# Kernel tuning notes

Hardware: AMD Instinct MI355X
Metric: run time of the kernel (lower is better)

## Reference

```python
import jax, jax.numpy as jnp
import numpy as np

T, D_IN, D_OUT, HEADS, FREQ = 2048, 1024, 1024, 8, 10000
DH = D_OUT // HEADS


def absolute_pos(t, d, freq):
    # AP[pos, 2i] = sin(pos / freq**(2i/d)), AP[pos, 2i+1] = cos(...); t even -> all cols filled
    pos = jnp.arange(t, dtype=jnp.float32)[:, None]            # [T,1]
    i = jnp.arange(t // 2, dtype=jnp.float32)[None, :]         # [1,T/2]
    angle = pos / (freq ** (2.0 * i / d))                      # [T,T/2]
    return jnp.stack([jnp.sin(angle), jnp.cos(angle)], axis=-1).reshape(t, t)


def setup_inputs() -> dict:
    key = jax.random.key(0)
    ks = jax.random.split(key, 6)
    s = 0.02
    return {
        "x": jax.random.normal(ks[0], (T, D_IN), jnp.float32),
        "Wq": jax.random.normal(ks[1], (HEADS, DH, D_IN), jnp.float32) * s,
        "Wk": jax.random.normal(ks[2], (HEADS, DH, D_IN), jnp.float32) * s,
        "Wv": jax.random.normal(ks[3], (HEADS, DH, D_IN), jnp.float32) * s,
        "Wout2": jax.random.normal(ks[4], (DH, DH + 2), jnp.float32) * s,
        "Wout": jax.random.normal(ks[5], (D_IN, D_OUT), jnp.float32) * s,
    }


def reference(x, Wq, Wk, Wv, Wout2, Wout):
    t = x.shape[0]
    # diversity = 1 - cosine similarity (F.normalize with eps=1e-12)
    x_unit = x / jnp.maximum(jnp.linalg.norm(x, axis=1, keepdims=True), 1e-12)
    diversity = 1.0 - x_unit @ x_unit.T                        # [T,T]

    # all heads vectorized; torch Linear weight is [out,in] -> x @ W.T
    Q = jnp.einsum('td,hed->hte', x, Wq)                       # [H,T,DH]
    K = jnp.einsum('td,hed->hte', x, Wk)
    V = jnp.einsum('td,hed->hte', x, Wv)

    AP = absolute_pos(t, D_IN, FREQ)                           # [T,T]
    energies = jnp.einsum('hte,hse->hts', Q, K) + AP           # [H,T,T]

    att = jax.nn.softmax(energies, axis=-1)
    logp = jax.nn.log_softmax(energies, axis=-1)
    entropy = -(att * logp).sum(-1) / np.float32(np.log(t))    # [H,T]
    entropy = entropy / jnp.maximum(jnp.abs(entropy).sum(-1, keepdims=True), 1e-12)

    # dep_factor[j] broadcast over rows: masked[i,j] = dep[j]*att[i,j]
    dep = (diversity[None] * att).sum(-1) / diversity.sum(-1)[None]  # [H,T]
    att_win = att + dep[:, None, :] * att                      # [H,T,T]

    # dropout(p=0.5) treated as identity (eval mode)
    y = jnp.einsum('hts,hse->hte', att_win, V)                 # [H,T,DH]

    chars = jax.lax.stop_gradient(jnp.stack([entropy, dep], axis=-1))  # [H,T,2]
    y_s = jnp.einsum('htf,of->hto', jnp.concatenate([y, chars], axis=-1), Wout2)  # [H,T,DH]

    y_cat = jnp.transpose(y_s, (1, 0, 2)).reshape(t, D_OUT)    # cat heads along feature dim
    out = y_cat @ Wout.T                                       # [T,D_IN]
    return out, att_win[-1]
```

## Files before the change

### kernel.cpp

```cpp
#include <hip/hip_runtime.h>
#include <math.h>

#define TT  2048
#define NH  8
#define DH  128
#define LNT 7.6246189861593985f

typedef unsigned short ushort_t;
typedef __bf16 bf16x8 __attribute__((ext_vector_type(8)));
typedef _Float16 f16x8 __attribute__((ext_vector_type(8)));
typedef float f32x4 __attribute__((ext_vector_type(4)));
typedef unsigned int uintx4 __attribute__((ext_vector_type(4)));

#define MFMA16(a, b, c)  __builtin_amdgcn_mfma_f32_16x16x32_bf16(a, b, c, 0, 0, 0)
#define MFMA16F(a, b, c) __builtin_amdgcn_mfma_f32_16x16x32_f16(a, b, c, 0, 0, 0)

__device__ __forceinline__ bf16x8 ld8(const ushort_t* p) {
  uintx4 v = *(const uintx4*)p;
  return __builtin_bit_cast(bf16x8, v);
}
__device__ __forceinline__ f16x8 ld8f(const ushort_t* p) {
  uintx4 v = *(const uintx4*)p;
  return __builtin_bit_cast(f16x8, v);
}
__device__ __forceinline__ ushort_t f2bf(float x) {
  unsigned u = __float_as_uint(x);
  return (ushort_t)((u + 0x7fffu + ((u >> 16) & 1u)) >> 16);
}
__device__ __forceinline__ float bf2f(ushort_t b) {
  return __uint_as_float(((unsigned)b) << 16);
}
__device__ __forceinline__ ushort_t f2h(float x) {
  return __builtin_bit_cast(ushort_t, (_Float16)x);
}
__device__ __forceinline__ float h2f(ushort_t b) {
  return (float)__builtin_bit_cast(_Float16, b);
}


enum : size_t {
  F_XF   = 0u,
  F_UF   = 1048576u,
  F_QF   = 2097152u,
  F_KF   = 3145728u,
  F_VBF  = 4194304u,
  F_VT   = 5242880u,
  F_YCF  = 6291456u,
  F_WCAT = 7340032u,
  F_WOF  = 9437184u,
  F_DIVS = 9961472u,
  F_LST  = 9979904u,
  F_ENTR = 9996288u,
  F_ENT  = 10012672u,
  F_DEP  = 10029056u,
  F_W2F  = 10307584u,
  F_APH  = 10485760u,
  F_C    = 12582912u,
  F_LP   = 6291456u,
  F_SAP  = 6422528u,
  F_SCP  = 6553600u,
  F_E    = 16777216u,
  F_YPALL= 33554432u,
  F_YSH  = 2097152u,
};

__device__ __forceinline__ float blockReduceSum256(float v) {
  __shared__ float sh[4];
  #pragma unroll
  for (int m = 1; m < 64; m <<= 1) v += __shfl_xor(v, m, 64);
  if ((threadIdx.x & 63) == 0) sh[threadIdx.x >> 6] = v;
  __syncthreads();
  float r = sh[0] + sh[1] + sh[2] + sh[3];
  __syncthreads();
  return r;
}

__global__ __launch_bounds__(256) void k_pre(
    const float* __restrict__ x, const float* __restrict__ Wq,
    const float* __restrict__ Wk, const float* __restrict__ Wv,
    const float* __restrict__ Wo, const float* __restrict__ W2,
    ushort_t* __restrict__ xf, ushort_t* __restrict__ Wcat,
    ushort_t* __restrict__ Wof, ushort_t* __restrict__ W2f,
    ushort_t* __restrict__ Uf, float* __restrict__ divsum) {
  int b = blockIdx.x;
  if (b < 4192) {
    int i = b * 256 + threadIdx.x;
    if (i < 1048576) {
      const float* src; ushort_t* dst; int j;
      if (i < 262144)       { src = Wq; dst = Wcat;           j = i; }
      else if (i < 524288)  { src = Wk; dst = Wcat + 1048576; j = i - 262144; }
      else if (i < 786432)  { src = Wv; dst = Wcat + 2097152; j = i - 524288; }
      else                  { src = Wo; dst = Wof;            j = i - 786432; }
      float4 v = ((const float4*)src)[j];
      uint2 w;
      w.x = (unsigned)f2h(v.x) | ((unsigned)f2h(v.y) << 16);
      w.y = (unsigned)f2h(v.z) | ((unsigned)f2h(v.w) << 16);
      ((uint2*)dst)[j] = w;
    } else {
      int idx = i - 1048576;
      int o = idx / 192, c = idx % 192;
      W2f[idx] = (c < 130) ? f2h(W2[o * 130 + c]) : (ushort_t)0;
    }
  } else if (b < 6240) {
    int t = b - 4192;
    const float* xr = x + (size_t)t * 1024;
    float ss = 0.f;
    for (int d = threadIdx.x; d < 1024; d += 256) { float v = xr[d]; ss += v * v; }
    ss = blockReduceSum256(ss);
    float inv = 1.f / fmaxf(sqrtf(ss), 1e-12f);
    for (int d = threadIdx.x; d < 1024; d += 256) {
      float v = xr[d];
      Uf[(size_t)t * 1024 + d] = f2h(v * inv);
      xf[(size_t)t * 1024 + d] = f2h(v);
    }
  } else {
    int idx = (b - 6240) * 256 + threadIdx.x;
    if (idx < TT) divsum[idx] = (float)TT;
  }
}

template <int MODE>
__device__ __forceinline__ void gemm_tile(
    ushort_t* As, ushort_t* Bs,
    const ushort_t* A, const ushort_t* B,
    float* Df, ushort_t* Dh,
    int M, int N, int K, int m0, int n0) {
  int tid = threadIdx.x, lane = tid & 63, w = tid >> 6;
  int l15 = lane & 15, lg = lane >> 4;
  int wr = w >> 1, wc = w & 1;

  const ushort_t* ga[4];
  const ushort_t* gb[4];
  ushort_t* la[4];
  ushort_t* lb[4];
  #pragma unroll
  for (int j = 0; j < 4; j++) {
    int u = (4 * w + j) * 64 + lane;
    int row = u >> 3;
    int kc8 = (u & 7) ^ (row & 7);
    ga[j] = A + (size_t)(m0 + row) * K + kc8 * 8;
    gb[j] = B + (size_t)(n0 + row) * K + kc8 * 8;
    la[j] = As + (4 * w + j) * 512;
    lb[j] = Bs + (4 * w + j) * 512;
  }

  f32x4 acc[4][4];
  #pragma unroll
  for (int i = 0; i < 4; i++)
    #pragma unroll
    for (int ct = 0; ct < 4; ct++) acc[i][ct] = (f32x4)0.f;

  for (int k0 = 0; k0 < K; k0 += 64) {
    __syncthreads();
    #pragma unroll
    for (int j = 0; j < 4; j++) {
      __builtin_amdgcn_global_load_lds(
          (const __attribute__((address_space(1))) void*)(ga[j] + k0),
          (__attribute__((address_space(3))) void*)la[j], 16, 0, 0);
      __builtin_amdgcn_global_load_lds(
          (const __attribute__((address_space(1))) void*)(gb[j] + k0),
          (__attribute__((address_space(3))) void*)lb[j], 16, 0, 0);
    }
    __syncthreads();
    #pragma unroll
    for (int kc = 0; kc < 2; kc++) {
      f16x8 af[4], bfr[4];
      #pragma unroll
      for (int i = 0; i < 4; i++) {
        int ra = wr * 64 + i * 16 + l15;
        af[i] = ld8f(As + (ra * 8 + ((kc * 4 + lg) ^ (ra & 7))) * 8);
        int rb = wc * 64 + i * 16 + l15;
        bfr[i] = ld8f(Bs + (rb * 8 + ((kc * 4 + lg) ^ (rb & 7))) * 8);
      }
      #pragma unroll
      for (int i = 0; i < 4; i++)
        #pragma unroll
        for (int ct = 0; ct < 4; ct++)
          acc[i][ct] = MFMA16F(af[i], bfr[ct], acc[i][ct]);
    }
  }
  if (MODE == 7) {
    #pragma unroll
    for (int i = 0; i < 4; i++) {
      float rs[4] = {0.f, 0.f, 0.f, 0.f};
      #pragma unroll
      for (int ct = 0; ct < 4; ct++) {
        size_t tile_t = (size_t)(m0 + wr * 64 + i * 16) >> 4;
        size_t tile_s = (size_t)(n0 + wc * 64 + ct * 16) >> 4;
        uint2 wv;
        wv.x = (unsigned)f2bf(acc[i][ct][0]) | ((unsigned)f2bf(acc[i][ct][1]) << 16);
        wv.y = (unsigned)f2bf(acc[i][ct][2]) | ((unsigned)f2bf(acc[i][ct][3]) << 16);
        *(uint2*)(Dh + (tile_t * (size_t)(N >> 4) + tile_s) * 256 + lg * 64 + l15 * 4) = wv;
        rs[0] += acc[i][ct][0]; rs[1] += acc[i][ct][1];
        rs[2] += acc[i][ct][2]; rs[3] += acc[i][ct][3];
      }
      #pragma unroll
      for (int r = 0; r < 4; r++) {
        float s = rs[r];
        s += __shfl_xor(s, 1, 64); s += __shfl_xor(s, 2, 64);
        s += __shfl_xor(s, 4, 64); s += __shfl_xor(s, 8, 64);
        if (l15 == 0)
          atomicAdd(&Df[m0 + wr * 64 + i * 16 + lg * 4 + r], -s);
      }
    }
    if (m0 != n0) {
      #pragma unroll
      for (int ct = 0; ct < 4; ct++) {
        float cs = 0.f;
        #pragma unroll
        for (int i = 0; i < 4; i++)
          #pragma unroll
          for (int r = 0; r < 4; r++) cs += acc[i][ct][r];
        cs += __shfl_xor(cs, 16, 64);
        cs += __shfl_xor(cs, 32, 64);
        if (lane < 16)
          atomicAdd(&Df[n0 + wc * 64 + ct * 16 + l15], -cs);
      }
      #pragma unroll
      for (int i = 0; i < 4; i++) {
        #pragma unroll
        for (int ct = 0; ct < 4; ct++) {
          size_t mbase = (((size_t)(n0 + wc * 64 + ct * 16) >> 4) * (size_t)(N >> 4)
                          + ((size_t)(m0 + wr * 64 + i * 16) >> 4)) * 256;
          #pragma unroll
          for (int r = 0; r < 4; r++)
            Dh[mbase + (l15 >> 2) * 64 + (lg * 4 + r) * 4 + (l15 & 3)] =
                f2bf(acc[i][ct][r]);
        }
      }
    }
  }
}

template <int MODE>
__device__ __forceinline__ void gemm64(
    ushort_t* As, ushort_t* Bs,
    const ushort_t* A, const ushort_t* B,
    float* Df, ushort_t* Dh,
    ushort_t* Dq, ushort_t* Dk, ushort_t* Dv,
    int N, int K, int m0, int n0) {
  int tid = threadIdx.x, lane = tid & 63, w = tid >> 6;
  int l15 = lane & 15, lg = lane >> 4;
  int wc = w;

  const ushort_t* gaA[2];
  ushort_t* laA[2];
  #pragma unroll
  for (int j = 0; j < 2; j++) {
    int u = (2 * w + j) * 64 + lane;
    int row = u >> 3;
    int kc8 = (u & 7) ^ (row & 7);
    gaA[j] = A + (size_t)(m0 + row) * K + kc8 * 8;
    laA[j] = As + (2 * w + j) * 512;
  }
  const ushort_t* gb[4];
  ushort_t* lb[4];
  #pragma unroll
  for (int j = 0; j < 4; j++) {
    int u = (4 * w + j) * 64 + lane;
    int row = u >> 3;
    int kc8 = (u & 7) ^ (row & 7);
    gb[j] = B + (size_t)(n0 + row) * K + kc8 * 8;
    lb[j] = Bs + (4 * w + j) * 512;
  }

  f32x4 acc[4][2];
  #pragma unroll
  for (int i = 0; i < 4; i++)
    #pragma unroll
    for (int ct = 0; ct < 2; ct++) acc[i][ct] = (f32x4)0.f;

  for (int k0 = 0; k0 < K; k0 += 64) {
    __syncthreads();
    #pragma unroll
    for (int j = 0; j < 2; j++)
      __builtin_amdgcn_global_load_lds(
          (const __attribute__((address_space(1))) void*)(gaA[j] + k0),
          (__attribute__((address_space(3))) void*)laA[j], 16, 0, 0);
    #pragma unroll
    for (int j = 0; j < 4; j++)
      __builtin_amdgcn_global_load_lds(
          (const __attribute__((address_space(1))) void*)(gb[j] + k0),
          (__attribute__((address_space(3))) void*)lb[j], 16, 0, 0);
    __syncthreads();
    #pragma unroll
    for (int kc = 0; kc < 2; kc++) {
      f16x8 af[4], bfr[2];
      #pragma unroll
      for (int i = 0; i < 4; i++) {
        int ra = i * 16 + l15;
        af[i] = ld8f(As + (ra * 8 + ((kc * 4 + lg) ^ (ra & 7))) * 8);
      }
      #pragma unroll
      for (int ct = 0; ct < 2; ct++) {
        int rb = wc * 32 + ct * 16 + l15;
        bfr[ct] = ld8f(Bs + (rb * 8 + ((kc * 4 + lg) ^ (rb & 7))) * 8);
      }
      #pragma unroll
      for (int i = 0; i < 4; i++)
        #pragma unroll
        for (int ct = 0; ct < 2; ct++)
          acc[i][ct] = MFMA16F(af[i], bfr[ct], acc[i][ct]);
    }
  }
  #pragma unroll
  for (int i = 0; i < 4; i++) {
    #pragma unroll
    for (int ct = 0; ct < 2; ct++) {
      #pragma unroll
      for (int r = 0; r < 4; r++) {
        size_t mm = m0 + i * 16 + lg * 4 + r;
        size_t nn = n0 + wc * 32 + ct * 16 + l15;
        float v = acc[i][ct][r];
        if (MODE == 0) Df[mm * N + nn] = v;
        if (MODE == 3) {
          if (nn < 1024) Dq[mm * 1024 + nn] = f2h(v);
          else if (nn < 2048) Dk[mm * 1024 + nn - 1024] = f2h(v);
          else Dv[mm * 1024 + nn - 2048] = f2bf(v);
        }
        if (MODE == 4) {
          size_t hh = mm >> 11, tt2 = mm & 2047;
          Dh[tt2 * 1024 + hh * 128 + nn] = f2h(v);
        }
      }
    }
  }
}

template <int MODE>
__global__ __launch_bounds__(256) void k_gemm64(
    const ushort_t* __restrict__ A, const ushort_t* __restrict__ B,
    float* __restrict__ Df, ushort_t* __restrict__ Dh,
    int N, int K) {
  __shared__ __align__(16) ushort_t As[64 * 64];
  __shared__ __align__(16) ushort_t Bs[128 * 64];
  gemm64<MODE>(As, Bs, A, B, Df, Dh, nullptr, nullptr, nullptr,
               N, K, blockIdx.y * 64, blockIdx.x * 128);
}

__global__ __launch_bounds__(256) void k_cqkv(
    const ushort_t* __restrict__ Uf, const ushort_t* __restrict__ xf,
    const ushort_t* __restrict__ Wcat,
    ushort_t* __restrict__ Cf, ushort_t* __restrict__ Qf,
    ushort_t* __restrict__ Kf, ushort_t* __restrict__ Vbf,
    float* __restrict__ divsum, ushort_t* __restrict__ APf) {
  __shared__ __align__(16) ushort_t As[128 * 64];
  __shared__ __align__(16) ushort_t Bs[128 * 64];
  int bid = blockIdx.x;
  if (bid < 136) {
    int rem = bid, bt = 0;
    while (rem >= 16 - bt) { rem -= 16 - bt; ++bt; }
    int bs = bt + rem;
    gemm_tile<7>(As, Bs, Uf, Uf, divsum, Cf,
                 TT, TT, 1024, bt * 128, bs * 128);
  } else if (bid < 904) {
    int b = bid - 136;
    gemm64<3>(As, Bs, xf, Wcat, nullptr, nullptr, Qf, Kf, Vbf,
              3072, 1024, (b / 24) * 64, (b % 24) * 128);
  } else {
    int bb = bid - 904;
    int tile_t = bb >> 4, sub = bb & 15;
    int base = sub * 2048;
    for (int u0 = threadIdx.x; u0 < 2048; u0 += 256) {
      int u = base + u0;
      int tile_s = u >> 8, slot = u & 255;
      int lg = slot >> 6, l15 = (slot >> 2) & 15, r = slot & 3;
      int t = tile_t * 16 + lg * 4 + r;
      int s = tile_s * 16 + l15;
      int i = s >> 1;
      float invf = __expf((float)i * -0.017988946039016016f);
      float ang = (float)t * invf;
      APf[(size_t)tile_t * 32768 + u] = f2h((s & 1) ? cosf(ang) : sinf(ang));
    }
  }
}

__global__ __launch_bounds__(512, 4) void k_phase1m(
    const ushort_t* __restrict__ Qf, const ushort_t* __restrict__ Kf,
    const ushort_t* __restrict__ APf, const ushort_t* __restrict__ Cf,
    ushort_t* __restrict__ Ef,
    float* __restrict__ Lp, float* __restrict__ sap, float* __restrict__ scp) {
  int h = blockIdx.y, z = blockIdx.z;
  int tid = threadIdx.x, lane = tid & 63, w = tid >> 6;
  int l15 = lane & 15, lg = lane >> 4;
  int rowbase = blockIdx.x * 128 + w * 16;
  int s_begin = z * 256, s_end = s_begin + 256;
  __shared__ __align__(16) ushort_t Ks[64 * 128];

  f16x8 q[4];
  {
    const ushort_t* qp = Qf + (size_t)(rowbase + l15) * 1024 + h * DH + lg * 8;
    #pragma unroll
    for (int kc = 0; kc < 4; kc++) q[kc] = ld8f(qp + kc * 32);
  }
  const ushort_t* apb = APf + (size_t)(rowbase >> 4) * 32768 + lane * 4;
  const ushort_t* cfb = Cf  + (size_t)(rowbase >> 4) * 32768 + lane * 4;
  ushort_t* eb = Ef + ((size_t)(h * 128 + (rowbase >> 4)) * 128) * 256 + lane * 4;

  int n0 = w * 128 + lane;
  int sr0 = n0 >> 4, su0 = n0 & 15, sr1 = sr0 + 4;
  int wo0 = sr0 * 128 + ((su0 ^ (sr0 & 7)) * 8);
  int wo1 = sr1 * 128 + ((su0 ^ (sr1 & 7)) * 8);
  const ushort_t* kg0 = Kf + (size_t)sr0 * 1024 + h * DH + su0 * 8;
  const ushort_t* kg1 = Kf + (size_t)sr1 * 1024 + h * DH + su0 * 8;

  float Lv[4], sae[4], snc[4];
  #pragma unroll
  for (int r = 0; r < 4; r++) { Lv[r] = 0.f; sae[r] = 0.f; snc[r] = 0.f; }

  uintx4 ka = *(const uintx4*)(kg0 + (size_t)s_begin * 1024);
  uintx4 kb = *(const uintx4*)(kg1 + (size_t)s_begin * 1024);

  for (int s0 = s_begin; s0 < s_end; s0 += 64) {
    int ts0 = s0 >> 4;
    f32x4 acc[4];
    float cc[4][4];
    #pragma unroll
    for (int ct = 0; ct < 4; ct++) {
      uint2 ap2 = *(const uint2*)(apb + (size_t)(ts0 + ct) * 256);
      uint2 c2  = *(const uint2*)(cfb + (size_t)(ts0 + ct) * 256);
      acc[ct][0] = h2f((ushort_t)(ap2.x & 0xffffu));
      acc[ct][1] = h2f((ushort_t)(ap2.x >> 16));
      acc[ct][2] = h2f((ushort_t)(ap2.y & 0xffffu));
      acc[ct][3] = h2f((ushort_t)(ap2.y >> 16));
      cc[ct][0] = bf2f((ushort_t)(c2.x & 0xffffu));
      cc[ct][1] = bf2f((ushort_t)(c2.x >> 16));
      cc[ct][2] = bf2f((ushort_t)(c2.y & 0xffffu));
      cc[ct][3] = bf2f((ushort_t)(c2.y >> 16));
    }
    __syncthreads();
    *(uintx4*)(Ks + wo0) = ka;
    *(uintx4*)(Ks + wo1) = kb;
    int s1 = s0 + 64;
    if (s1 < s_end) {
      ka = *(const uintx4*)(kg0 + (size_t)s1 * 1024);
      kb = *(const uintx4*)(kg1 + (size_t)s1 * 1024);
    }
    __syncthreads();
    #pragma unroll
    for (int ct = 0; ct < 4; ct++) {
      int row = ct * 16 + l15, rb = row * 128, rsw = row & 7;
      #pragma unroll
      for (int kc = 0; kc < 4; kc++) {
        f16x8 b = ld8f(Ks + rb + (((kc * 4 + lg) ^ rsw) * 8));
        acc[ct] = MFMA16F(q[kc], b, acc[ct]);
      }
    }
    #pragma unroll
    for (int ct = 0; ct < 4; ct++) {
      uint2 ev;
      ev.x = (unsigned)f2h(acc[ct][0]) | ((unsigned)f2h(acc[ct][1]) << 16);
      ev.y = (unsigned)f2h(acc[ct][2]) | ((unsigned)f2h(acc[ct][3]) << 16);
      *(uint2*)(eb + (size_t)(ts0 + ct) * 256) = ev;
    }
    #pragma unroll
    for (int r = 0; r < 4; r++) {
      float e0 = acc[0][r], e1 = acc[1][r], e2 = acc[2][r], e3 = acc[3][r];
      float p0 = __expf(e0), p1 = __expf(e1), p2 = __expf(e2), p3 = __expf(e3);
      Lv[r]  += (p0 + p1) + (p2 + p3);
      sae[r] += (p0 * e0 + p1 * e1) + (p2 * e2 + p3 * e3);
      snc[r] += (p0 * cc[0][r] + p1 * cc[1][r]) + (p2 * cc[2][r] + p3 * cc[3][r]);
    }
  }
  #pragma unroll
  for (int r = 0; r < 4; r++) {
    #pragma unroll
    for (int m = 1; m < 16; m <<= 1) {
      Lv[r]  += __shfl_xor(Lv[r], m, 64);
      sae[r] += __shfl_xor(sae[r], m, 64);
      snc[r] += __shfl_xor(snc[r], m, 64);
    }
  }
  if (l15 == 0) {
    #pragma unroll
    for (int r = 0; r < 4; r++) {
      int t = rowbase + lg * 4 + r;
      size_t idx = (size_t)z * (NH * TT) + h * TT + t;
      Lp[idx] = Lv[r]; sap[idx] = sae[r]; scp[idx] = snc[r];
    }
  }
}

__global__ __launch_bounds__(256) void k_combine(
    const float* __restrict__ Lp, const float* __restrict__ sap,
    const float* __restrict__ scp, const float* __restrict__ divsum,
    float* __restrict__ Lst, float* __restrict__ entraw, float* __restrict__ dep) {
  int i = blockIdx.x * 256 + threadIdx.x;
  if (i >= NH * TT) return;
  float L = 0.f, sa = 0.f, sc = 0.f;
  #pragma unroll
  for (int c = 0; c < 8; c++) {
    size_t idx = (size_t)c * (NH * TT) + i;
    L += Lp[idx]; sa += sap[idx]; sc += scp[idx];
  }
  float logL = __logf(L);
  Lst[i] = logL;
  entraw[i] = (logL - sa / L) * (1.0f / LNT);
  int t = i & (TT - 1);
  dep[i] = (1.f - sc / L) / divsum[t];
}

__global__ __launch_bounds__(256) void k_entvp(
    const float* __restrict__ entraw, float* __restrict__ ent,
    const ushort_t* __restrict__ Vbf, const float* __restrict__ dep,
    ushort_t* __restrict__ VT) {
  __shared__ float tile[64][130];
  int b = blockIdx.x;
  if (b < 8) {
    int h = b;
    float s = 0.f;
    for (int t = threadIdx.x; t < TT; t += 256) s += fabsf(entraw[h * TT + t]);
    s = blockReduceSum256(s);
    float inv = 1.f / fmaxf(s, 1e-12f);
    for (int t = threadIdx.x; t < TT; t += 256)
      ent[h * TT + t] = entraw[h * TT + t] * inv;
  } else {
    int bb = b - 8;
    int h = bb >> 5, s0 = (bb & 31) * 64;
    int tid = threadIdx.x;
    for (int idx = tid; idx < 64 * 64; idx += 256) {
      int r = idx >> 6, c2 = (idx & 63) * 2;
      unsigned u = *(const unsigned*)&Vbf[(size_t)(s0 + r) * 1024 + h * DH + c2];
      tile[r][c2] = bf2f((ushort_t)(u & 0xffffu));
      tile[r][c2 + 1] = bf2f((ushort_t)(u >> 16));
    }
    __syncthreads();
    int e = tid >> 1, sh = (tid & 1) * 32;
    #pragma unroll
    for (int g = 0; g < 8; g++) {
      int sb = sh + g * 4;
      float v0 = tile[sb + 0][e] * (1.f + dep[h * TT + s0 + sb + 0]);
      float v1 = tile[sb + 1][e] * (1.f + dep[h * TT + s0 + sb + 1]);
      float v2 = tile[sb + 2][e] * (1.f + dep[h * TT + s0 + sb + 2]);
      float v3 = tile[sb + 3][e] * (1.f + dep[h * TT + s0 + sb + 3]);
      uint2 wv;
      wv.x = (unsigned)f2bf(v0) | ((unsigned)f2bf(v1) << 16);
      wv.y = (unsigned)f2bf(v2) | ((unsigned)f2bf(v3) << 16);
      *(uint2*)&VT[(size_t)(h * DH + e) * TT + s0 + sb] = wv;
    }
  }
}

__global__ __launch_bounds__(512, 4) void k_phase2m(
    const ushort_t* __restrict__ Ef, const ushort_t* __restrict__ VT,
    const float* __restrict__ Lst, const float* __restrict__ dep,
    ushort_t* __restrict__ ypall, float* __restrict__ out2) {
  int h = (blockIdx.y + 7) & 7;
  int z = blockIdx.z;
  int tid = threadIdx.x, lane = tid & 63, w = tid >> 6;
  int l15 = lane & 15, lg = lane >> 4;
  int rowbase = blockIdx.x * 128 + w * 16;
  bool last = (h == NH - 1);
  int s_begin = z * 256, s_end = s_begin + 256;
  ushort_t* yp = ypall + (size_t)z * 2097152;

  __shared__ __align__(16) ushort_t Vs[128 * 64];
  __shared__ __align__(16) ushort_t Pst[8][16][72];

  float ml[4];
  #pragma unroll
  for (int r = 0; r < 4; r++) ml[r] = Lst[h * TT + rowbase + lg * 4 + r];
  const ushort_t* eb = Ef + ((size_t)(h * 128 + (rowbase >> 4)) * 128) * 256 + lane * 4;

  int n0 = w * 128 + lane;
  int ve0 = n0 >> 3, vu0 = n0 & 7;
  int vwo0 = ve0 * 64 + ((vu0 ^ (ve0 & 7)) * 8);
  int vwo1 = vwo0 + 512;
  const ushort_t* vg0 = VT + (size_t)(h * DH + ve0) * TT + vu0 * 8;
  const ushort_t* vg1 = vg0 + (size_t)8 * TT;

  f32x4 yacc[8];
  #pragma unroll
  for (int et = 0; et < 8; et++) yacc[et] = (f32x4)0.f;

  uintx4 va = *(const uintx4*)(vg0 + s_begin);
  uintx4 vb = *(const uintx4*)(vg1 + s_begin);

  for (int s0 = s_begin; s0 < s_end; s0 += 64) {
    int ts0 = s0 >> 4;
    uint2 e2[4];
    #pragma unroll
    for (int ct = 0; ct < 4; ct++)
      e2[ct] = *(const uint2*)(eb + (size_t)(ts0 + ct) * 256);
    __syncthreads();
    *(uintx4*)(Vs + vwo0) = va;
    *(uintx4*)(Vs + vwo1) = vb;
    int s1 = s0 + 64;
    if (s1 < s_end) {
      va = *(const uintx4*)(vg0 + s1);
      vb = *(const uintx4*)(vg1 + s1);
    }
    __syncthreads();
    float dv[4];
    if (last) {
      #pragma unroll
      for (int ct = 0; ct < 4; ct++) dv[ct] = dep[(NH - 1) * TT + s0 + ct * 16 + l15];
    }
    #pragma unroll
    for (int ct = 0; ct < 4; ct++) {
      float e0 = h2f((ushort_t)(e2[ct].x & 0xffffu));
      float e1 = h2f((ushort_t)(e2[ct].x >> 16));
      float e3 = h2f((ushort_t)(e2[ct].y & 0xffffu));
      float e4 = h2f((ushort_t)(e2[ct].y >> 16));
      float a0 = __expf(e0 - ml[0]);
      float a1 = __expf(e1 - ml[1]);
      float a2 = __expf(e3 - ml[2]);
      float a3 = __expf(e4 - ml[3]);
      Pst[w][lg * 4 + 0][ct * 16 + l15] = f2bf(a0);
      Pst[w][lg * 4 + 1][ct * 16 + l15] = f2bf(a1);
      Pst[w][lg * 4 + 2][ct * 16 + l15] = f2bf(a2);
      Pst[w][lg * 4 + 3][ct * 16 + l15] = f2bf(a3);
      if (last) {
        float sc = 1.f + dv[ct];
        out2[(size_t)(rowbase + lg * 4 + 0) * TT + s0 + ct * 16 + l15] = a0 * sc;
        out2[(size_t)(rowbase + lg * 4 + 1) * TT + s0 + ct * 16 + l15] = a1 * sc;
        out2[(size_t)(rowbase + lg * 4 + 2) * TT + s0 + ct * 16 + l15] = a2 * sc;
        out2[(size_t)(rowbase + lg * 4 + 3) * TT + s0 + ct * 16 + l15] = a3 * sc;
      }
    }
    asm volatile("" ::: "memory");
    #pragma unroll
    for (int c = 0; c < 2; c++) {
      bf16x8 ap = *(const bf16x8*)&Pst[w][l15][c * 32 + lg * 8];
      #pragma unroll
      for (int et = 0; et < 8; et++) {
        int e = et * 16 + l15;
        bf16x8 bv = ld8(Vs + e * 64 + (((c * 4 + lg) ^ (l15 & 7)) * 8));
        yacc[et] = MFMA16(ap, bv, yacc[et]);
      }
    }
    asm volatile("" ::: "memory");
  }
  #pragma unroll
  for (int et = 0; et < 8; et++)
    #pragma unroll
    for (int r = 0; r < 4; r++)
      yp[((size_t)h * TT + rowbase + lg * 4 + r) * DH + et * 16 + l15] = f2h(yacc[et][r]);
}

__device__ __forceinline__ void acc8(const ushort_t* p, float* s) {
  uintx4 v = *(const uintx4*)p;
  #pragma unroll
  for (int q = 0; q < 4; q++) {
    s[q * 2]     += h2f((ushort_t)(v[q] & 0xffffu));
    s[q * 2 + 1] += h2f((ushort_t)(v[q] >> 16));
  }
}
__global__ __launch_bounds__(256) void k_ysum(
    const ushort_t* __restrict__ ypall,
    const float* __restrict__ ent, const float* __restrict__ dep,
    ushort_t* __restrict__ ysh) {
  int i = blockIdx.x * 256 + threadIdx.x;
  int g = i & 15, t = (i >> 4) & 2047, h = i >> 15;
  size_t src = ((size_t)h * TT + t) * DH + g * 8;
  float s[8];
  #pragma unroll
  for (int q = 0; q < 8; q++) s[q] = 0.f;
  #pragma unroll
  for (int b = 0; b < 8; b++) acc8(ypall + (size_t)b * 2097152 + src, s);
  uintx4 o;
  o[0] = (unsigned)f2h(s[0]) | ((unsigned)f2h(s[1]) << 16);
  o[1] = (unsigned)f2h(s[2]) | ((unsigned)f2h(s[3]) << 16);
  o[2] = (unsigned)f2h(s[4]) | ((unsigned)f2h(s[5]) << 16);
  o[3] = (unsigned)f2h(s[6]) | ((unsigned)f2h(s[7]) << 16);
  ushort_t* row = ysh + ((size_t)h * TT + t) * 192;
  *(uintx4*)(row + g * 8) = o;
  if (g == 0) {
    uint2 cz;
    cz.x = (unsigned)f2h(ent[h * TT + t]) | ((unsigned)f2h(dep[h * TT + t]) << 16);
    cz.y = 0u;
    *(uint2*)(row + 128) = cz;
    uint2 z2; z2.x = 0u; z2.y = 0u;
    #pragma unroll
    for (int q = 132; q < 192; q += 4) *(uint2*)(row + q) = z2;
  }
}

extern "C" void kernel_launch(void* const* d_in, const int* in_sizes, int n_in,
                              void* d_out, int out_size, void* d_ws, size_t ws_size,
                              hipStream_t stream) {
  const float* x  = (const float*)d_in[0];
  const float* Wq = (const float*)d_in[1];
  const float* Wk = (const float*)d_in[2];
  const float* Wv = (const float*)d_in[3];
  const float* W2 = (const float*)d_in[4];
  const float* Wo = (const float*)d_in[5];
  float* out  = (float*)d_out;
  float* out2 = out + (size_t)TT * 1024;
  float* ws = (float*)d_ws;

  ushort_t* xf   = (ushort_t*)(ws + F_XF);
  ushort_t* Uf   = (ushort_t*)(ws + F_UF);
  ushort_t* Qf   = (ushort_t*)(ws + F_QF);
  ushort_t* Kf   = (ushort_t*)(ws + F_KF);
  ushort_t* Vbf  = (ushort_t*)(ws + F_VBF);
  ushort_t* VT   = (ushort_t*)(ws + F_VT);
  ushort_t* ycf  = (ushort_t*)(ws + F_YCF);
  ushort_t* Wcat = (ushort_t*)(ws + F_WCAT);
  ushort_t* Wof  = (ushort_t*)(ws + F_WOF);
  ushort_t* W2f  = (ushort_t*)(ws + F_W2F);
  ushort_t* APf  = (ushort_t*)(ws + F_APH);
  ushort_t* ysh  = (ushort_t*)(ws + F_YSH);
  ushort_t* Cf   = (ushort_t*)(ws + F_C);
  ushort_t* Ef   = (ushort_t*)(ws + F_E);
  ushort_t* ypall= (ushort_t*)(ws + F_YPALL);
  float* divsum = ws + F_DIVS;
  float* Lst    = ws + F_LST;
  float* entraw = ws + F_ENTR;
  float* ent    = ws + F_ENT;
  float* dep    = ws + F_DEP;
  float* Lp     = ws + F_LP;
  float* sap    = ws + F_SAP;
  float* scp    = ws + F_SCP;

  k_pre<<<6248, 256, 0, stream>>>(x, Wq, Wk, Wv, Wo, W2,
                                  xf, Wcat, Wof, W2f, Uf, divsum);
  k_cqkv<<<2952, 256, 0, stream>>>(Uf, xf, Wcat, Cf, Qf, Kf, Vbf, divsum, APf);

  k_phase1m<<<dim3(16, NH, 8), 512, 0, stream>>>(Qf, Kf, APf, Cf, Ef, Lp, sap, scp);
  k_combine<<<64, 256, 0, stream>>>(Lp, sap, scp, divsum, Lst, entraw, dep);
  k_entvp<<<264, 256, 0, stream>>>(entraw, ent, Vbf, dep, VT);
  k_phase2m<<<dim3(16, NH, 8), 512, 0, stream>>>(Ef, VT, Lst, dep, ypall, out2);
  k_ysum<<<1024, 256, 0, stream>>>(ypall, ent, dep, ysh);
  k_gemm64<4><<<dim3(1, 256), 256, 0, stream>>>(ysh, W2f, nullptr, ycf, 128, 192);
  k_gemm64<0><<<dim3(8, 32), 256, 0, stream>>>(ycf, Wof, out, nullptr, 1024, 1024);
}
```

Baseline: 153.6 us.

## Double-buffer LDS tiles in gemm64 to overlap global loads with MFMA

The 64x128 GEMM path (QKV projection inside k_cqkv and the standalone k_gemm64) now uses two LDS buffers per operand. It prefetches the next K-slice with global_load_lds while MFMAs run on the current slice, and uses one barrier per iteration instead of two. The aim is to hide global-to-LDS latency behind compute. In exchange, LDS use per block rises (k_cqkv goes to 48KB), which can lower occupancy. The shared buffers are also re-laid out so that gemm_tile still sees contiguous regions.

```diff
diff --git a/kernel.cpp b/kernel.cpp
--- a/kernel.cpp
+++ b/kernel.cpp
@@ -14,6 +14,10 @@
 
 #define MFMA16(a, b, c)  __builtin_amdgcn_mfma_f32_16x16x32_bf16(a, b, c, 0, 0, 0)
 #define MFMA16F(a, b, c) __builtin_amdgcn_mfma_f32_16x16x32_f16(a, b, c, 0, 0, 0)
+
+#define GLL(gp, lp) __builtin_amdgcn_global_load_lds(                        \
+    (const __attribute__((address_space(1))) void*)(gp),                     \
+    (__attribute__((address_space(3))) void*)(lp), 16, 0, 0)
 
 __device__ __forceinline__ bf16x8 ld8(const ushort_t* p) {
   uintx4 v = *(const uintx4*)p;
@@ -154,12 +158,8 @@
     __syncthreads();
     #pragma unroll
     for (int j = 0; j < 4; j++) {
-      __builtin_amdgcn_global_load_lds(
-          (const __attribute__((address_space(1))) void*)(ga[j] + k0),
-          (__attribute__((address_space(3))) void*)la[j], 16, 0, 0);
-      __builtin_amdgcn_global_load_lds(
-          (const __attribute__((address_space(1))) void*)(gb[j] + k0),
-          (__attribute__((address_space(3))) void*)lb[j], 16, 0, 0);
+      GLL(ga[j] + k0, la[j]);
+      GLL(gb[j] + k0, lb[j]);
     }
     __syncthreads();
     #pragma unroll
@@ -234,7 +234,7 @@
 
 template <int MODE>
 __device__ __forceinline__ void gemm64(
-    ushort_t* As, ushort_t* Bs,
+    ushort_t* As0, ushort_t* As1, ushort_t* Bs0, ushort_t* Bs1,
     const ushort_t* A, const ushort_t* B,
     float* Df, ushort_t* Dh,
     ushort_t* Dq, ushort_t* Dk, ushort_t* Dv,
@@ -244,24 +244,24 @@
   int wc = w;
 
   const ushort_t* gaA[2];
-  ushort_t* laA[2];
+  int laOff[2];
   #pragma unroll
   for (int j = 0; j < 2; j++) {
     int u = (2 * w + j) * 64 + lane;
     int row = u >> 3;
     int kc8 = (u & 7) ^ (row & 7);
     gaA[j] = A + (size_t)(m0 + row) * K + kc8 * 8;
-    laA[j] = As + (2 * w + j) * 512;
+    laOff[j] = (2 * w + j) * 512;
   }
   const ushort_t* gb[4];
-  ushort_t* lb[4];
+  int lbOff[4];
   #pragma unroll
   for (int j = 0; j < 4; j++) {
     int u = (4 * w + j) * 64 + lane;
     int row = u >> 3;
     int kc8 = (u & 7) ^ (row & 7);
     gb[j] = B + (size_t)(n0 + row) * K + kc8 * 8;
-    lb[j] = Bs + (4 * w + j) * 512;
+    lbOff[j] = (4 * w + j) * 512;
   }
 
   f32x4 acc[4][2];
@@ -270,31 +270,37 @@
     #pragma unroll
     for (int ct = 0; ct < 2; ct++) acc[i][ct] = (f32x4)0.f;
 
+  #pragma unroll
+  for (int j = 0; j < 2; j++) GLL(gaA[j], As0 + laOff[j]);
+  #pragma unroll
+  for (int j = 0; j < 4; j++) GLL(gb[j], Bs0 + lbOff[j]);
+  __syncthreads();
+
+  int cur = 0;
   for (int k0 = 0; k0 < K; k0 += 64) {
-    __syncthreads();
-    #pragma unroll
-    for (int j = 0; j < 2; j++)
-      __builtin_amdgcn_global_load_lds(
-          (const __attribute__((address_space(1))) void*)(gaA[j] + k0),
-          (__attribute__((address_space(3))) void*)laA[j], 16, 0, 0);
-    #pragma unroll
-    for (int j = 0; j < 4; j++)
-      __builtin_amdgcn_global_load_lds(
-          (const __attribute__((address_space(1))) void*)(gb[j] + k0),
-          (__attribute__((address_space(3))) void*)lb[j], 16, 0, 0);
-    __syncthreads();
+    ushort_t* Ac = cur ? As1 : As0;
+    ushort_t* Bc = cur ? Bs1 : Bs0;
+    int k1 = k0 + 64;
+    if (k1 < K) {
+      ushort_t* An = cur ? As0 : As1;
+      ushort_t* Bn = cur ? Bs0 : Bs1;
+      #pragma unroll
+      for (int j = 0; j < 2; j++) GLL(gaA[j] + k1, An + laOff[j]);
+      #pragma unroll
+      for (int j = 0; j < 4; j++) GLL(gb[j] + k1, Bn + lbOff[j]);
+    }
     #pragma unroll
     for (int kc = 0; kc < 2; kc++) {
       f16x8 af[4], bfr[2];
       #pragma unroll
       for (int i = 0; i < 4; i++) {
         int ra = i * 16 + l15;
-        af[i] = ld8f(As + (ra * 8 + ((kc * 4 + lg) ^ (ra & 7))) * 8);
+        af[i] = ld8f(Ac + (ra * 8 + ((kc * 4 + lg) ^ (ra & 7))) * 8);
       }
       #pragma unroll
       for (int ct = 0; ct < 2; ct++) {
         int rb = wc * 32 + ct * 16 + l15;
-        bfr[ct] = ld8f(Bs + (rb * 8 + ((kc * 4 + lg) ^ (rb & 7))) * 8);
+        bfr[ct] = ld8f(Bc + (rb * 8 + ((kc * 4 + lg) ^ (rb & 7))) * 8);
       }
       #pragma unroll
       for (int i = 0; i < 4; i++)
@@ -302,6 +308,8 @@
         for (int ct = 0; ct < 2; ct++)
           acc[i][ct] = MFMA16F(af[i], bfr[ct], acc[i][ct]);
     }
+    __syncthreads();
+    cur ^= 1;
   }
   #pragma unroll
   for (int i = 0; i < 4; i++) {
@@ -332,9 +340,10 @@
     const ushort_t* __restrict__ A, const ushort_t* __restrict__ B,
     float* __restrict__ Df, ushort_t* __restrict__ Dh,
     int N, int K) {
-  __shared__ __align__(16) ushort_t As[64 * 64];
-  __shared__ __align__(16) ushort_t Bs[128 * 64];
-  gemm64<MODE>(As, Bs, A, B, Df, Dh, nullptr, nullptr, nullptr,
+  __shared__ __align__(16) ushort_t SA[2][64 * 64];
+  __shared__ __align__(16) ushort_t SB[2][128 * 64];
+  gemm64<MODE>(SA[0], SA[1], SB[0], SB[1], A, B, Df, Dh,
+               nullptr, nullptr, nullptr,
                N, K, blockIdx.y * 64, blockIdx.x * 128);
 }
 
@@ -344,19 +353,19 @@
     ushort_t* __restrict__ Cf, ushort_t* __restrict__ Qf,
     ushort_t* __restrict__ Kf, ushort_t* __restrict__ Vbf,
     float* __restrict__ divsum, ushort_t* __restrict__ APf) {
-  __shared__ __align__(16) ushort_t As[128 * 64];
-  __shared__ __align__(16) ushort_t Bs[128 * 64];
+  __shared__ __align__(16) ushort_t SA[2][64 * 64];
+  __shared__ __align__(16) ushort_t SB[2][128 * 64];
   int bid = blockIdx.x;
   if (bid < 136) {
     int rem = bid, bt = 0;
     while (rem >= 16 - bt) { rem -= 16 - bt; ++bt; }
     int bs = bt + rem;
-    gemm_tile<7>(As, Bs, Uf, Uf, divsum, Cf,
+    gemm_tile<7>(&SA[0][0], &SB[0][0], Uf, Uf, divsum, Cf,
                  TT, TT, 1024, bt * 128, bs * 128);
   } else if (bid < 904) {
     int b = bid - 136;
-    gemm64<3>(As, Bs, xf, Wcat, nullptr, nullptr, Qf, Kf, Vbf,
-              3072, 1024, (b / 24) * 64, (b % 24) * 128);
+    gemm64<3>(SA[0], SA[1], SB[0], SB[1], xf, Wcat, nullptr, nullptr,
+              Qf, Kf, Vbf, 3072, 1024, (b / 24) * 64, (b % 24) * 128);
   } else {
     int bb = bid - 904;
     int tile_t = bb >> 4, sub = bb & 15;
```

Measured after the change: 147.5 us. 1.04x faster.
